# Performance work log

Hardware: AMD Instinct MI355X
Metric: run time of the kernel (lower is better)

## Reference

```python
import jax, jax.numpy as jnp
import numpy as np
from jax import lax

WINDOW_SIZE = 5
SIGMA = 1.0
DILATIONS = [1 + int(i ** 1.5) for i in range(5)]  # [1, 2, 3, 6, 9]
C1 = (0.01 * 255.0) ** 2
C2 = (0.03 * 255.0) ** 2


def _make_window(channel=1):
    x = np.arange(WINDOW_SIZE, dtype=np.float64)
    g = np.exp(-((x - WINDOW_SIZE // 2) ** 2) / (2.0 * SIGMA ** 2))
    g = g / g.sum()
    w2d = np.outer(g, g)
    w2d = w2d / w2d.sum()
    w = np.broadcast_to(w2d[None, None], (channel, 1, WINDOW_SIZE, WINDOW_SIZE))
    return jnp.asarray(w, jnp.float32)


def _dw_conv(x, window, dilation):
    # depthwise 'same' conv; pad = (dilated_kernel - 1)/2 = 2*dilation (always even total pad)
    pad = 2 * dilation
    return lax.conv_general_dilated(
        x, window, window_strides=(1, 1),
        padding=((pad, pad), (pad, pad)),
        rhs_dilation=(dilation, dilation),
        dimension_numbers=('NCHW', 'OIHW', 'NCHW'),
        feature_group_count=window.shape[0])


def _ssim_mean(img1, img2, window, dilation):
    mu1 = _dw_conv(img1, window, dilation)
    mu2 = _dw_conv(img2, window, dilation)
    si11 = _dw_conv(img1 * img1, window, dilation)
    si22 = _dw_conv(img2 * img2, window, dilation)
    si12 = _dw_conv(img1 * img2, window, dilation)
    mu1_sq = mu1 * mu1
    mu2_sq = mu2 * mu2
    mu1_mu2 = mu1 * mu2
    sigma1_sq = si11 - mu1_sq
    sigma2_sq = si22 - mu2_sq
    sigma12 = si12 - mu1_mu2
    ssim_map = ((2.0 * mu1_mu2 + C1) * (2.0 * sigma12 + C2)) / (
        (mu1_sq + mu2_sq + C1) * (sigma1_sq + sigma2_sq + C2))
    return jnp.mean(ssim_map)


def _avg_pool2(x):
    B, C, H, W = x.shape
    return x.reshape(B, C, H // 2, 2, W // 2, 2).mean(axis=(3, 5))


def setup_inputs() -> dict:
    key = jax.random.key(0)
    k1, k2 = jax.random.split(key)
    img1 = jax.random.uniform(k1, (16, 1, 1024, 1024), dtype=jnp.float32)
    img2 = jax.random.uniform(k2, (16, 1, 1024, 1024), dtype=jnp.float32)
    window = _make_window(channel=1)
    weights = jnp.asarray([0.0448, 0.2856, 0.3001, 0.2363, 0.1333], jnp.float32)
    return {"img1": img1, "img2": img2, "window": window, "weights": weights}


def reference(img1, img2, window, weights):
    eps = 1e-12
    m = jnp.max(img2)
    a = (img1 + eps) / (m + eps) * 255.0
    b = (img2 + eps) / (m + eps) * 255.0
    mssim = []
    for dil in DILATIONS:
        mssim.append(_ssim_mean(a, b, window, dil))
        a = _avg_pool2(a)
        b = _avg_pool2(b)
    mssim = jnp.stack(mssim)
    return 1.0 - jnp.prod(mssim ** weights)
```

## Files before the change

### kernel.cpp

```cpp
#include <hip/hip_runtime.h>
#include <math.h>

#define EPSN 1e-12f
#define SSIM_C1 6.5025f
#define SSIM_C2 58.5225f


typedef __attribute__((ext_vector_type(2))) float vf2;

__global__ void init_ws_kernel(float* ws) {
    if (threadIdx.x < 16) ws[threadIdx.x] = 0.0f;
}

__global__ void max_kernel(const float4* __restrict__ img2, int n4,
                           unsigned* __restrict__ maxbits) {
    float m = 0.0f;
    for (int i = blockIdx.x * blockDim.x + threadIdx.x; i < n4;
         i += gridDim.x * blockDim.x) {
        float4 v = img2[i];
        m = fmaxf(fmaxf(m, fmaxf(v.x, v.y)), fmaxf(v.z, v.w));
    }
#pragma unroll
    for (int o = 32; o > 0; o >>= 1) m = fmaxf(m, __shfl_down(m, o));
    __shared__ float sm[4];
    int tid = threadIdx.x;
    if ((tid & 63) == 0) sm[tid >> 6] = m;
    __syncthreads();
    if (tid == 0) {
        float mm = fmaxf(fmaxf(sm[0], sm[1]), fmaxf(sm[2], sm[3]));
        atomicMax(maxbits, __float_as_uint(mm));
    }
}


template <int D, bool RAW>
__global__ __launch_bounds__(256) void ssim_sep_kernel(
        const float* __restrict__ A, const float* __restrict__ B,
        int H, int W, const unsigned* __restrict__ maxbits,
        const float* __restrict__ window, float* __restrict__ sumOut,
        vf2* __restrict__ poolPM) {
    constexpr int TW = 64, TH = 64, TPT = 16;
    constexpr int LW = TW + 4 * D, LH = TH + 4 * D;
    __shared__ vf2 AB[LH][LW];

    int tx = threadIdx.x, ty = threadIdx.y;
    int tid = ty * 64 + tx;
    int b = blockIdx.z;
    int x0i = blockIdx.x * TW;
    int y0 = blockIdx.y * TH - 2 * D;

    if (RAW) {
        const float* Ab = A + (size_t)b * H * W;
        const float* Bb = B + (size_t)b * H * W;
        for (int idx = tid; idx < LH * 16; idx += 256) {
            int ly = idx >> 4, j = idx & 15;
            int gy = y0 + ly;
            float4 a = make_float4(0, 0, 0, 0), v = make_float4(0, 0, 0, 0);
            if ((unsigned)gy < (unsigned)H) {
                a = *(const float4*)(Ab + (size_t)gy * W + x0i + 4 * j);
                v = *(const float4*)(Bb + (size_t)gy * W + x0i + 4 * j);
            }
            float4 lo = make_float4(a.x + v.x, a.x - v.x, a.y + v.y, a.y - v.y);
            float4 hi = make_float4(a.z + v.z, a.z - v.z, a.w + v.w, a.w - v.w);
            int sig = ((j >> 2) ^ j) & 1;
            float4* rowp = (float4*)(&AB[ly][0]);
            rowp[D + 2 * j + sig] = sig ? hi : lo;
            rowp[D + 2 * j + 1 - sig] = sig ? lo : hi;
        }
        for (int idx = tid; idx < LH * 4 * D; idx += 256) {
            int ly = idx / (4 * D), h = idx % (4 * D);
            int lx = (h < 2 * D) ? h : h + TW;
            int gx = x0i - 2 * D + lx;
            int gy = y0 + ly;
            vf2 pm = {0.0f, 0.0f};
            if ((unsigned)gx < (unsigned)W && (unsigned)gy < (unsigned)H) {
                size_t g = (size_t)gy * W + gx;
                float a = Ab[g], v = Bb[g];
                pm = vf2{a + v, a - v};
            }
            AB[ly][lx] = pm;
        }
    } else {
        const vf2* pmIn = (const vf2*)A;
        const vf2* base = pmIn + (size_t)b * H * W;
        for (int idx = tid; idx < LH * 32; idx += 256) {
            int ly = idx >> 5, j = idx & 31;
            int gy = y0 + ly;
            float4 g = make_float4(0, 0, 0, 0);
            if ((unsigned)gy < (unsigned)H)
                g = *(const float4*)(base + (size_t)gy * W + x0i + 2 * j);
            ((float4*)&AB[ly][0])[D + j] = g;
        }
        for (int idx = tid; idx < LH * 4 * D; idx += 256) {
            int ly = idx / (4 * D), h = idx % (4 * D);
            int lx = (h < 2 * D) ? h : h + TW;
            int gx = x0i - 2 * D + lx;
            int gy = y0 + ly;
            vf2 pm = {0.0f, 0.0f};
            if ((unsigned)gx < (unsigned)W && (unsigned)gy < (unsigned)H)
                pm = base[(size_t)gy * W + gx];
            AB[ly][lx] = pm;
        }
    }
    __syncthreads();

    if (poolPM) {
        int pW = W >> 1;
        for (int idx = tid; idx < 32 * 16; idx += 256) {
            int py = idx >> 4, j2 = idx & 15;
            int sx = 2 * D + 4 * j2, sy = 2 * D + 2 * py;
            vf2 s00 = AB[sy][sx],     s01 = AB[sy][sx + 1];
            vf2 s10 = AB[sy + 1][sx], s11 = AB[sy + 1][sx + 1];
            vf2 o0 = 0.25f * ((s00 + s01) + (s10 + s11));
            vf2 t00 = AB[sy][sx + 2],     t01 = AB[sy][sx + 3];
            vf2 t10 = AB[sy + 1][sx + 2], t11 = AB[sy + 1][sx + 3];
            vf2 o1 = 0.25f * ((t00 + t01) + (t10 + t11));
            int gx = (x0i >> 1) + 2 * j2;
            int gy = ((blockIdx.y * TH) >> 1) + py;
            float4 o = make_float4(o0.x, o0.y, o1.x, o1.y);
            *(float4*)(poolPM + (size_t)b * (H >> 1) * pW + (size_t)gy * pW + gx) = o;
        }
    }

    float g1[5];
#pragma unroll
    for (int k = 0; k < 5; k++)
        g1[k] = ((window[k * 5 + 0] + window[k * 5 + 1]) +
                 (window[k * 5 + 2] + window[k * 5 + 3])) + window[k * 5 + 4];

    float mx = __uint_as_float(*maxbits);
    float sc = 255.0f / (mx + EPSN);
    float s2h = 0.5f * sc * sc;

    vf2 rPM[5], rSQ[5];
    float local = 0.0f;
    int rbase = ty * TPT;

#pragma unroll
    for (int ph = 0; ph < D; ++ph) {
        const int cnt = (TPT - ph + D - 1) / D;
#pragma unroll
        for (int k = 0; k < cnt + 4; ++k) {
            int l = rbase + ph + k * D;
            vf2 hpm = {0.0f, 0.0f}, hsq = {0.0f, 0.0f};
#pragma unroll
            for (int kt = 0; kt < 5; kt++) {
                vf2 ab = AB[l][tx + kt * D];
                vf2 wab = g1[kt] * ab;
                hpm += wab;
                hsq += wab * ab;
            }
            rPM[k % 5] = hpm;
            rSQ[k % 5] = hsq;
            if (k >= 4) {
                vf2 vpm = {0.0f, 0.0f}, vsq = {0.0f, 0.0f};
#pragma unroll
                for (int kt = 0; kt < 5; kt++) {
                    int sl = (k - 4 + kt) % 5;
                    vpm += g1[kt] * rPM[sl];
                    vsq += g1[kt] * rSQ[sl];
                }
                float u = vpm.x * vpm.x, vv = vpm.y * vpm.y;
                float upv = u + vv, umv = u - vv;
                float qp = vsq.x + vsq.y, qm = vsq.x - vsq.y;
                float num1 = fmaf(s2h, umv, SSIM_C1);
                float den1 = fmaf(s2h, upv, SSIM_C1);
                float num2 = fmaf(s2h, qm - umv, SSIM_C2);
                float den2 = fmaf(s2h, qp - upv, SSIM_C2);
                local += (num1 * num2) * __builtin_amdgcn_rcpf(den1 * den2);
            }
        }
    }

#pragma unroll
    for (int o = 32; o > 0; o >>= 1) local += __shfl_down(local, o);
    __shared__ float part[4];
    if ((tid & 63) == 0) part[tid >> 6] = local;
    __syncthreads();
    if (tid == 0) atomicAdd(sumOut, (part[0] + part[1]) + (part[2] + part[3]));
}


template <int D, int TH>
__global__ __launch_bounds__(256) void ssim_direct_kernel(
        const vf2* __restrict__ pmIn, int H, int W,
        const unsigned* __restrict__ maxbits,
        const float* __restrict__ window, float* __restrict__ sumOut,
        vf2* __restrict__ poolPM) {
    constexpr int TW = 64;
    constexpr int LW = TW + 4 * D, LH = TH + 4 * D, OPT = TH / 4;
    __shared__ vf2 AB[LH][LW];

    int tx = threadIdx.x, ty = threadIdx.y;
    int tid = ty * 64 + tx;
    int b = blockIdx.z;
    int x0i = blockIdx.x * TW;
    int y0 = blockIdx.y * TH - 2 * D;
    const vf2* base = pmIn + (size_t)b * H * W;

    for (int idx = tid; idx < LH * 32; idx += 256) {
        int ly = idx >> 5, j = idx & 31;
        int gy = y0 + ly;
        float4 g = make_float4(0, 0, 0, 0);
        if ((unsigned)gy < (unsigned)H)
            g = *(const float4*)(base + (size_t)gy * W + x0i + 2 * j);
        ((float4*)&AB[ly][0])[D + j] = g;
    }
    for (int idx = tid; idx < LH * 4 * D; idx += 256) {
        int ly = idx / (4 * D), h = idx % (4 * D);
        int lx = (h < 2 * D) ? h : h + TW;
        int gx = x0i - 2 * D + lx;
        int gy = y0 + ly;
        vf2 pm = {0.0f, 0.0f};
        if ((unsigned)gx < (unsigned)W && (unsigned)gy < (unsigned)H)
            pm = base[(size_t)gy * W + gx];
        AB[ly][lx] = pm;
    }
    __syncthreads();

    if (poolPM) {
        int pW = W >> 1;
        for (int idx = tid; idx < 16 * (TH / 2); idx += 256) {
            int py = idx >> 4, j2 = idx & 15;
            int sx = 2 * D + 4 * j2, sy = 2 * D + 2 * py;
            vf2 s00 = AB[sy][sx],     s01 = AB[sy][sx + 1];
            vf2 s10 = AB[sy + 1][sx], s11 = AB[sy + 1][sx + 1];
            vf2 o0 = 0.25f * ((s00 + s01) + (s10 + s11));
            vf2 t00 = AB[sy][sx + 2],     t01 = AB[sy][sx + 3];
            vf2 t10 = AB[sy + 1][sx + 2], t11 = AB[sy + 1][sx + 3];
            vf2 o1 = 0.25f * ((t00 + t01) + (t10 + t11));
            int gx = (x0i >> 1) + 2 * j2;
            int gy = ((blockIdx.y * TH) >> 1) + py;
            float4 o = make_float4(o0.x, o0.y, o1.x, o1.y);
            *(float4*)(poolPM + (size_t)b * (H >> 1) * pW + (size_t)gy * pW + gx) = o;
        }
    }

    float wv[25];
#pragma unroll
    for (int i = 0; i < 25; i++) wv[i] = window[i];

    float mx = __uint_as_float(*maxbits);
    float sc = 255.0f / (mx + EPSN);
    float s2h = 0.5f * sc * sc;

    vf2 mu[OPT], sq[OPT];
#pragma unroll
    for (int j = 0; j < OPT; j++) { mu[j] = vf2{0, 0}; sq[j] = vf2{0, 0}; }
    int ry = ty * OPT;
#pragma unroll
    for (int ky = 0; ky < 5; ky++) {
#pragma unroll
        for (int kx = 0; kx < 5; kx++) {
            float w = wv[ky * 5 + kx];
#pragma unroll
            for (int j = 0; j < OPT; j++) {
                vf2 ab = AB[ry + j + ky * D][tx + kx * D];
                vf2 wab = w * ab;
                mu[j] += wab;
                sq[j] += wab * ab;
            }
        }
    }

    float local = 0.0f;
#pragma unroll
    for (int j = 0; j < OPT; j++) {
        float u = mu[j].x * mu[j].x, vv = mu[j].y * mu[j].y;
        float upv = u + vv, umv = u - vv;
        float qp = sq[j].x + sq[j].y, qm = sq[j].x - sq[j].y;
        float num1 = fmaf(s2h, umv, SSIM_C1);
        float den1 = fmaf(s2h, upv, SSIM_C1);
        float num2 = fmaf(s2h, qm - umv, SSIM_C2);
        float den2 = fmaf(s2h, qp - upv, SSIM_C2);
        local += (num1 * num2) * __builtin_amdgcn_rcpf(den1 * den2);
    }

#pragma unroll
    for (int o = 32; o > 0; o >>= 1) local += __shfl_down(local, o);
    __shared__ float part[4];
    if ((tid & 63) == 0) part[tid >> 6] = local;
    __syncthreads();
    if (tid == 0) atomicAdd(sumOut, (part[0] + part[1]) + (part[2] + part[3]));
}


__global__ void final_kernel(const float* __restrict__ sums,
                             const float* __restrict__ weights,
                             unsigned* __restrict__ out) {
    if (blockIdx.x == 0 && threadIdx.x == 0) {
        const float counts[5] = {16.0f * 1024 * 1024, 16.0f * 512 * 512,
                                 16.0f * 256 * 256,   16.0f * 128 * 128,
                                 16.0f * 64 * 64};
        float prod = 1.0f;
#pragma unroll
        for (int i = 0; i < 5; i++) {
            float m = sums[i] / counts[i];
            prod *= powf(m, weights[i]);
        }
        float r = 1.0f - prod;
        unsigned bits = __float_as_uint(r);
        unsigned lsb = (bits >> 16) & 1u;
        unsigned hi = (bits + 0x7FFFu + lsb) >> 16;
        out[0] = (hi << 16) | hi;
    }
}


extern "C" void kernel_launch(void* const* d_in, const int* in_sizes, int n_in,
                              void* d_out, int out_size, void* d_ws, size_t ws_size,
                              hipStream_t stream) {
    const float* img1 = (const float*)d_in[0];
    const float* img2 = (const float*)d_in[1];
    const float* window = (const float*)d_in[2];
    const float* weights = (const float*)d_in[3];

    float* ws = (float*)d_ws;
    unsigned* maxbits = (unsigned*)d_ws;
    float* sums = ws + 4;
    size_t off = 16;
    vf2* pm1 = (vf2*)(ws + off); off += (size_t)16 * 512 * 512 * 2;
    vf2* pm2 = (vf2*)(ws + off); off += (size_t)16 * 256 * 256 * 2;
    vf2* pm3 = (vf2*)(ws + off); off += (size_t)16 * 128 * 128 * 2;
    vf2* pm4 = (vf2*)(ws + off); off += (size_t)16 * 64 * 64 * 2;

    dim3 blk(64, 4, 1);

    init_ws_kernel<<<1, 64, 0, stream>>>(ws);
    max_kernel<<<2048, 256, 0, stream>>>((const float4*)img2,
                                         16 * 1024 * 1024 / 4, maxbits);

    ssim_sep_kernel<1, true><<<dim3(16, 16, 16), blk, 0, stream>>>(
        img1, img2, 1024, 1024, maxbits, window, sums + 0, pm1);
    ssim_sep_kernel<2, false><<<dim3(8, 8, 16), blk, 0, stream>>>(
        (const float*)pm1, nullptr, 512, 512, maxbits, window, sums + 1, pm2);
    ssim_sep_kernel<3, false><<<dim3(4, 4, 16), blk, 0, stream>>>(
        (const float*)pm2, nullptr, 256, 256, maxbits, window, sums + 2, pm3);
    ssim_direct_kernel<6, 8><<<dim3(2, 16, 16), blk, 0, stream>>>(
        pm3, 128, 128, maxbits, window, sums + 3, pm4);
    ssim_direct_kernel<9, 8><<<dim3(1, 8, 16), blk, 0, stream>>>(
        pm4, 64, 64, maxbits, window, sums + 4, nullptr);

    final_kernel<<<1, 64, 0, stream>>>(sums, weights, (unsigned*)d_out);
}
```

Baseline: 302.9 us.

## Fuse coarse SSIM levels into one tail kernel pooling directly from level-1 buffer

Levels 1–4 are merged into a single tail kernel whose block ranges dispatch per level, and coarser levels rebuild their pooled tiles directly from the level-1 pm buffer instead of reading intermediate pooled buffers written by earlier kernels. The max reduction now writes per-block partials that each consumer block reduces itself, and the init kernel is folded into the max kernel, which removes the atomicMax and two launches. This cuts kernel launches and serial dependencies between small levels, so the coarse levels can run concurrently. In exchange, coarse levels re-read and re-average more level-1 data per tile, and every block repeats the small partial-max reduction.

```diff
diff --git a/kernel.cpp b/kernel.cpp
--- a/kernel.cpp
+++ b/kernel.cpp
@@ -8,40 +8,71 @@
 
 typedef __attribute__((ext_vector_type(2))) float vf2;
 
-__global__ void init_ws_kernel(float* ws) {
-    if (threadIdx.x < 16) ws[threadIdx.x] = 0.0f;
-}
-
-__global__ void max_kernel(const float4* __restrict__ img2, int n4,
-                           unsigned* __restrict__ maxbits) {
+
+__global__ void max_part_kernel(const float4* __restrict__ img2, int n4,
+                                float* __restrict__ partials,
+                                float* __restrict__ sums) {
+    int tid = threadIdx.x;
+    if (blockIdx.x == 256) {
+        if (tid < 5) sums[tid] = 0.0f;
+        return;
+    }
     float m = 0.0f;
-    for (int i = blockIdx.x * blockDim.x + threadIdx.x; i < n4;
-         i += gridDim.x * blockDim.x) {
+    for (int i = blockIdx.x * 256 + tid; i < n4; i += 256 * 256) {
         float4 v = img2[i];
         m = fmaxf(fmaxf(m, fmaxf(v.x, v.y)), fmaxf(v.z, v.w));
     }
 #pragma unroll
     for (int o = 32; o > 0; o >>= 1) m = fmaxf(m, __shfl_down(m, o));
     __shared__ float sm[4];
-    int tid = threadIdx.x;
     if ((tid & 63) == 0) sm[tid >> 6] = m;
     __syncthreads();
-    if (tid == 0) {
-        float mm = fmaxf(fmaxf(sm[0], sm[1]), fmaxf(sm[2], sm[3]));
-        atomicMax(maxbits, __float_as_uint(mm));
-    }
-}
-
-
-template <int D, bool RAW>
-__global__ __launch_bounds__(256) void ssim_sep_kernel(
+    if (tid == 0)
+        partials[blockIdx.x] = fmaxf(fmaxf(sm[0], sm[1]), fmaxf(sm[2], sm[3]));
+}
+
+
+__device__ __forceinline__ float max_from_partials_start(
+        const float* __restrict__ partials, float* sm4, int tid) {
+    float mv = partials[tid & 255];
+#pragma unroll
+    for (int o = 32; o > 0; o >>= 1) mv = fmaxf(mv, __shfl_down(mv, o));
+    if ((tid & 63) == 0) sm4[tid >> 6] = mv;
+    return 0.0f;
+}
+
+__device__ __forceinline__ void block_sum_add(float local, float* part, int tid,
+                                              float* __restrict__ sumOut) {
+#pragma unroll
+    for (int o = 32; o > 0; o >>= 1) local += __shfl_down(local, o);
+    if ((tid & 63) == 0) part[tid >> 6] = local;
+    __syncthreads();
+    if (tid == 0)
+        atomicAdd(sumOut, (part[0] + part[1]) + (part[2] + part[3]));
+}
+
+__device__ __forceinline__ float ssim_px(vf2 vpm, vf2 vsq, float s2h) {
+    float u = vpm.x * vpm.x, vv = vpm.y * vpm.y;
+    float upv = u + vv, umv = u - vv;
+    float qp = vsq.x + vsq.y, qm = vsq.x - vsq.y;
+    float num1 = fmaf(s2h, umv, SSIM_C1);
+    float den1 = fmaf(s2h, upv, SSIM_C1);
+    float num2 = fmaf(s2h, qm - umv, SSIM_C2);
+    float den2 = fmaf(s2h, qp - upv, SSIM_C2);
+    return (num1 * num2) * __builtin_amdgcn_rcpf(den1 * den2);
+}
+
+
+__global__ __launch_bounds__(256) void ssim0_kernel(
         const float* __restrict__ A, const float* __restrict__ B,
-        int H, int W, const unsigned* __restrict__ maxbits,
-        const float* __restrict__ window, float* __restrict__ sumOut,
-        vf2* __restrict__ poolPM) {
-    constexpr int TW = 64, TH = 64, TPT = 16;
+        const float* __restrict__ window, const float* __restrict__ partials,
+        float* __restrict__ sums, vf2* __restrict__ poolPM) {
+    constexpr int D = 1, TW = 64, TH = 64, TPT = 16;
     constexpr int LW = TW + 4 * D, LH = TH + 4 * D;
+    const int H = 1024, W = 1024;
     __shared__ vf2 AB[LH][LW];
+    __shared__ float sm4[4];
+    __shared__ float part[4];
 
     int tx = threadIdx.x, ty = threadIdx.y;
     int tid = ty * 64 + tx;
@@ -49,70 +80,49 @@
     int x0i = blockIdx.x * TW;
     int y0 = blockIdx.y * TH - 2 * D;
 
-    if (RAW) {
-        const float* Ab = A + (size_t)b * H * W;
-        const float* Bb = B + (size_t)b * H * W;
-        for (int idx = tid; idx < LH * 16; idx += 256) {
-            int ly = idx >> 4, j = idx & 15;
-            int gy = y0 + ly;
-            float4 a = make_float4(0, 0, 0, 0), v = make_float4(0, 0, 0, 0);
-            if ((unsigned)gy < (unsigned)H) {
-                a = *(const float4*)(Ab + (size_t)gy * W + x0i + 4 * j);
-                v = *(const float4*)(Bb + (size_t)gy * W + x0i + 4 * j);
-            }
-            float4 lo = make_float4(a.x + v.x, a.x - v.x, a.y + v.y, a.y - v.y);
-            float4 hi = make_float4(a.z + v.z, a.z - v.z, a.w + v.w, a.w - v.w);
-            int sig = ((j >> 2) ^ j) & 1;
-            float4* rowp = (float4*)(&AB[ly][0]);
-            rowp[D + 2 * j + sig] = sig ? hi : lo;
-            rowp[D + 2 * j + 1 - sig] = sig ? lo : hi;
-        }
-        for (int idx = tid; idx < LH * 4 * D; idx += 256) {
-            int ly = idx / (4 * D), h = idx % (4 * D);
-            int lx = (h < 2 * D) ? h : h + TW;
-            int gx = x0i - 2 * D + lx;
-            int gy = y0 + ly;
-            vf2 pm = {0.0f, 0.0f};
-            if ((unsigned)gx < (unsigned)W && (unsigned)gy < (unsigned)H) {
-                size_t g = (size_t)gy * W + gx;
-                float a = Ab[g], v = Bb[g];
-                pm = vf2{a + v, a - v};
-            }
-            AB[ly][lx] = pm;
-        }
-    } else {
-        const vf2* pmIn = (const vf2*)A;
-        const vf2* base = pmIn + (size_t)b * H * W;
-        for (int idx = tid; idx < LH * 32; idx += 256) {
-            int ly = idx >> 5, j = idx & 31;
-            int gy = y0 + ly;
-            float4 g = make_float4(0, 0, 0, 0);
-            if ((unsigned)gy < (unsigned)H)
-                g = *(const float4*)(base + (size_t)gy * W + x0i + 2 * j);
-            ((float4*)&AB[ly][0])[D + j] = g;
-        }
-        for (int idx = tid; idx < LH * 4 * D; idx += 256) {
-            int ly = idx / (4 * D), h = idx % (4 * D);
-            int lx = (h < 2 * D) ? h : h + TW;
-            int gx = x0i - 2 * D + lx;
-            int gy = y0 + ly;
-            vf2 pm = {0.0f, 0.0f};
-            if ((unsigned)gx < (unsigned)W && (unsigned)gy < (unsigned)H)
-                pm = base[(size_t)gy * W + gx];
-            AB[ly][lx] = pm;
-        }
+    max_from_partials_start(partials, sm4, tid);
+
+    const float* Ab = A + (size_t)b * H * W;
+    const float* Bb = B + (size_t)b * H * W;
+    for (int idx = tid; idx < LH * 16; idx += 256) {
+        int ly = idx >> 4, j = idx & 15;
+        int gy = y0 + ly;
+        float4 a = make_float4(0, 0, 0, 0), v = make_float4(0, 0, 0, 0);
+        if ((unsigned)gy < (unsigned)H) {
+            a = *(const float4*)(Ab + (size_t)gy * W + x0i + 4 * j);
+            v = *(const float4*)(Bb + (size_t)gy * W + x0i + 4 * j);
+        }
+        float4 lo = make_float4(a.x + v.x, a.x - v.x, a.y + v.y, a.y - v.y);
+        float4 hi = make_float4(a.z + v.z, a.z - v.z, a.w + v.w, a.w - v.w);
+        int sig = ((j >> 2) ^ j) & 1;
+        float4* rowp = (float4*)(&AB[ly][0]);
+        rowp[D + 2 * j + sig] = sig ? hi : lo;
+        rowp[D + 2 * j + 1 - sig] = sig ? lo : hi;
+    }
+    for (int idx = tid; idx < LH * 4 * D; idx += 256) {
+        int ly = idx / (4 * D), h = idx % (4 * D);
+        int lx = (h < 2 * D) ? h : h + TW;
+        int gx = x0i - 2 * D + lx;
+        int gy = y0 + ly;
+        vf2 pm = {0.0f, 0.0f};
+        if ((unsigned)gx < (unsigned)W && (unsigned)gy < (unsigned)H) {
+            size_t g = (size_t)gy * W + gx;
+            float a = Ab[g], v = Bb[g];
+            pm = vf2{a + v, a - v};
+        }
+        AB[ly][lx] = pm;
     }
     __syncthreads();
 
-    if (poolPM) {
+    {
         int pW = W >> 1;
         for (int idx = tid; idx < 32 * 16; idx += 256) {
             int py = idx >> 4, j2 = idx & 15;
             int sx = 2 * D + 4 * j2, sy = 2 * D + 2 * py;
-            vf2 s00 = AB[sy][sx],     s01 = AB[sy][sx + 1];
+            vf2 s00 = AB[sy][sx], s01 = AB[sy][sx + 1];
             vf2 s10 = AB[sy + 1][sx], s11 = AB[sy + 1][sx + 1];
             vf2 o0 = 0.25f * ((s00 + s01) + (s10 + s11));
-            vf2 t00 = AB[sy][sx + 2],     t01 = AB[sy][sx + 3];
+            vf2 t00 = AB[sy][sx + 2], t01 = AB[sy][sx + 3];
             vf2 t10 = AB[sy + 1][sx + 2], t11 = AB[sy + 1][sx + 3];
             vf2 o1 = 0.25f * ((t00 + t01) + (t10 + t11));
             int gx = (x0i >> 1) + 2 * j2;
@@ -128,21 +138,110 @@
         g1[k] = ((window[k * 5 + 0] + window[k * 5 + 1]) +
                  (window[k * 5 + 2] + window[k * 5 + 3])) + window[k * 5 + 4];
 
-    float mx = __uint_as_float(*maxbits);
+    float mx = fmaxf(fmaxf(sm4[0], sm4[1]), fmaxf(sm4[2], sm4[3]));
     float sc = 255.0f / (mx + EPSN);
     float s2h = 0.5f * sc * sc;
 
     vf2 rPM[5], rSQ[5];
     float local = 0.0f;
     int rbase = ty * TPT;
-
+#pragma unroll
+    for (int k = 0; k < TPT + 4; ++k) {
+        int l = rbase + k;
+        vf2 hpm = {0, 0}, hsq = {0, 0};
+#pragma unroll
+        for (int kt = 0; kt < 5; kt++) {
+            vf2 ab = AB[l][tx + kt];
+            vf2 wab = g1[kt] * ab;
+            hpm += wab;
+            hsq += wab * ab;
+        }
+        rPM[k % 5] = hpm;
+        rSQ[k % 5] = hsq;
+        if (k >= 4) {
+            vf2 vpm = {0, 0}, vsq = {0, 0};
+#pragma unroll
+            for (int kt = 0; kt < 5; kt++) {
+                int sl = (k - 4 + kt) % 5;
+                vpm += g1[kt] * rPM[sl];
+                vsq += g1[kt] * rSQ[sl];
+            }
+            local += ssim_px(vpm, vsq, s2h);
+        }
+    }
+    block_sum_add(local, part, tid, sums + 0);
+}
+
+
+template <int D, int TH, int POOL>
+__device__ void sep_level(const vf2* __restrict__ base, const float* g1,
+                          int bx, int by, const float* sm4, float* part,
+                          float* __restrict__ sumOut, vf2* ldsRaw, int tid) {
+    constexpr int TW = 64, TPT = TH / 4;
+    constexpr int W = 512 / POOL;
+    constexpr int LW = TW + 4 * D, LH = TH + 4 * D;
+    vf2(*AB)[LW] = (vf2(*)[LW])ldsRaw;
+    int tx = tid & 63, ty = tid >> 6;
+    int x0i = bx * TW, y0 = by * TH - 2 * D;
+
+    if constexpr (POOL == 1) {
+        for (int idx = tid; idx < LH * 32; idx += 256) {
+            int ly = idx >> 5, j = idx & 31;
+            int gy = y0 + ly;
+            float4 g = make_float4(0, 0, 0, 0);
+            if ((unsigned)gy < (unsigned)W)
+                g = *(const float4*)(base + (size_t)gy * 512 + x0i + 2 * j);
+            ((float4*)&AB[ly][0])[D + j] = g;
+        }
+        for (int idx = tid; idx < LH * 4 * D; idx += 256) {
+            int ly = idx / (4 * D), h = idx % (4 * D);
+            int lx = (h < 2 * D) ? h : h + TW;
+            int gx = x0i - 2 * D + lx, gy = y0 + ly;
+            vf2 pm = {0, 0};
+            if ((unsigned)gx < (unsigned)W && (unsigned)gy < (unsigned)W)
+                pm = base[(size_t)gy * 512 + gx];
+            AB[ly][lx] = pm;
+        }
+    } else {
+        constexpr float inv = 1.0f / (POOL * POOL);
+        int px0 = x0i - 2 * D;
+        for (int idx = tid; idx < LW * LH; idx += 256) {
+            int ly = idx / LW, lx = idx - ly * LW;
+            int px = px0 + lx, py = y0 + ly;
+            vf2 acc = {0, 0};
+            if ((unsigned)px < (unsigned)W && (unsigned)py < (unsigned)W) {
+                const vf2* r0 = base + (size_t)(py * POOL) * 512 + px * POOL;
+#pragma unroll
+                for (int ry = 0; ry < POOL; ry++) {
+                    const float4* rp = (const float4*)(r0 + (size_t)ry * 512);
+#pragma unroll
+                    for (int rx = 0; rx < POOL / 2; rx++) {
+                        float4 v = rp[rx];
+                        acc.x += v.x + v.z;
+                        acc.y += v.y + v.w;
+                    }
+                }
+                acc *= inv;
+            }
+            AB[ly][lx] = acc;
+        }
+    }
+    __syncthreads();
+
+    float mx = fmaxf(fmaxf(sm4[0], sm4[1]), fmaxf(sm4[2], sm4[3]));
+    float sc = 255.0f / (mx + EPSN);
+    float s2h = 0.5f * sc * sc;
+
+    vf2 rPM[5], rSQ[5];
+    float local = 0.0f;
+    int rbase = ty * TPT;
 #pragma unroll
     for (int ph = 0; ph < D; ++ph) {
         const int cnt = (TPT - ph + D - 1) / D;
 #pragma unroll
         for (int k = 0; k < cnt + 4; ++k) {
             int l = rbase + ph + k * D;
-            vf2 hpm = {0.0f, 0.0f}, hsq = {0.0f, 0.0f};
+            vf2 hpm = {0, 0}, hsq = {0, 0};
 #pragma unroll
             for (int kt = 0; kt < 5; kt++) {
                 vf2 ab = AB[l][tx + kt * D];
@@ -153,135 +252,118 @@
             rPM[k % 5] = hpm;
             rSQ[k % 5] = hsq;
             if (k >= 4) {
-                vf2 vpm = {0.0f, 0.0f}, vsq = {0.0f, 0.0f};
+                vf2 vpm = {0, 0}, vsq = {0, 0};
 #pragma unroll
                 for (int kt = 0; kt < 5; kt++) {
                     int sl = (k - 4 + kt) % 5;
                     vpm += g1[kt] * rPM[sl];
                     vsq += g1[kt] * rSQ[sl];
                 }
-                float u = vpm.x * vpm.x, vv = vpm.y * vpm.y;
-                float upv = u + vv, umv = u - vv;
-                float qp = vsq.x + vsq.y, qm = vsq.x - vsq.y;
-                float num1 = fmaf(s2h, umv, SSIM_C1);
-                float den1 = fmaf(s2h, upv, SSIM_C1);
-                float num2 = fmaf(s2h, qm - umv, SSIM_C2);
-                float den2 = fmaf(s2h, qp - upv, SSIM_C2);
-                local += (num1 * num2) * __builtin_amdgcn_rcpf(den1 * den2);
-            }
-        }
-    }
-
-#pragma unroll
-    for (int o = 32; o > 0; o >>= 1) local += __shfl_down(local, o);
-    __shared__ float part[4];
-    if ((tid & 63) == 0) part[tid >> 6] = local;
+                local += ssim_px(vpm, vsq, s2h);
+            }
+        }
+    }
+    block_sum_add(local, part, tid, sumOut);
+}
+
+template <int D, int TW, int TH, int POOL>
+__device__ void direct_level(const vf2* __restrict__ base, const float* g1,
+                             int bx, int by, const float* sm4, float* part,
+                             float* __restrict__ sumOut, vf2* ldsRaw, int tid) {
+    constexpr int W = 512 / POOL;
+    constexpr int LW = TW + 4 * D, LH = TH + 4 * D;
+    constexpr int NOUT = TW * TH / 256;
+    constexpr float inv = 1.0f / (POOL * POOL);
+    vf2(*AB)[LW] = (vf2(*)[LW])ldsRaw;
+    int x0i = bx * TW, y0 = by * TH - 2 * D;
+    int px0 = x0i - 2 * D;
+
+    for (int idx = tid; idx < LW * LH; idx += 256) {
+        int ly = idx / LW, lx = idx - ly * LW;
+        int px = px0 + lx, py = y0 + ly;
+        vf2 acc = {0, 0};
+        if ((unsigned)px < (unsigned)W && (unsigned)py < (unsigned)W) {
+            const vf2* r0 = base + (size_t)(py * POOL) * 512 + px * POOL;
+#pragma unroll
+            for (int ry = 0; ry < POOL; ry++) {
+                const float4* rp = (const float4*)(r0 + (size_t)ry * 512);
+#pragma unroll
+                for (int rx = 0; rx < POOL / 2; rx++) {
+                    float4 v = rp[rx];
+                    acc.x += v.x + v.z;
+                    acc.y += v.y + v.w;
+                }
+            }
+            acc *= inv;
+        }
+        AB[ly][lx] = acc;
+    }
     __syncthreads();
-    if (tid == 0) atomicAdd(sumOut, (part[0] + part[1]) + (part[2] + part[3]));
-}
-
-
-template <int D, int TH>
-__global__ __launch_bounds__(256) void ssim_direct_kernel(
-        const vf2* __restrict__ pmIn, int H, int W,
-        const unsigned* __restrict__ maxbits,
-        const float* __restrict__ window, float* __restrict__ sumOut,
-        vf2* __restrict__ poolPM) {
-    constexpr int TW = 64;
-    constexpr int LW = TW + 4 * D, LH = TH + 4 * D, OPT = TH / 4;
-    __shared__ vf2 AB[LH][LW];
-
-    int tx = threadIdx.x, ty = threadIdx.y;
-    int tid = ty * 64 + tx;
-    int b = blockIdx.z;
-    int x0i = blockIdx.x * TW;
-    int y0 = blockIdx.y * TH - 2 * D;
-    const vf2* base = pmIn + (size_t)b * H * W;
-
-    for (int idx = tid; idx < LH * 32; idx += 256) {
-        int ly = idx >> 5, j = idx & 31;
-        int gy = y0 + ly;
-        float4 g = make_float4(0, 0, 0, 0);
-        if ((unsigned)gy < (unsigned)H)
-            g = *(const float4*)(base + (size_t)gy * W + x0i + 2 * j);
-        ((float4*)&AB[ly][0])[D + j] = g;
-    }
-    for (int idx = tid; idx < LH * 4 * D; idx += 256) {
-        int ly = idx / (4 * D), h = idx % (4 * D);
-        int lx = (h < 2 * D) ? h : h + TW;
-        int gx = x0i - 2 * D + lx;
-        int gy = y0 + ly;
-        vf2 pm = {0.0f, 0.0f};
-        if ((unsigned)gx < (unsigned)W && (unsigned)gy < (unsigned)H)
-            pm = base[(size_t)gy * W + gx];
-        AB[ly][lx] = pm;
-    }
-    __syncthreads();
-
-    if (poolPM) {
-        int pW = W >> 1;
-        for (int idx = tid; idx < 16 * (TH / 2); idx += 256) {
-            int py = idx >> 4, j2 = idx & 15;
-            int sx = 2 * D + 4 * j2, sy = 2 * D + 2 * py;
-            vf2 s00 = AB[sy][sx],     s01 = AB[sy][sx + 1];
-            vf2 s10 = AB[sy + 1][sx], s11 = AB[sy + 1][sx + 1];
-            vf2 o0 = 0.25f * ((s00 + s01) + (s10 + s11));
-            vf2 t00 = AB[sy][sx + 2],     t01 = AB[sy][sx + 3];
-            vf2 t10 = AB[sy + 1][sx + 2], t11 = AB[sy + 1][sx + 3];
-            vf2 o1 = 0.25f * ((t00 + t01) + (t10 + t11));
-            int gx = (x0i >> 1) + 2 * j2;
-            int gy = ((blockIdx.y * TH) >> 1) + py;
-            float4 o = make_float4(o0.x, o0.y, o1.x, o1.y);
-            *(float4*)(poolPM + (size_t)b * (H >> 1) * pW + (size_t)gy * pW + gx) = o;
-        }
-    }
-
-    float wv[25];
-#pragma unroll
-    for (int i = 0; i < 25; i++) wv[i] = window[i];
-
-    float mx = __uint_as_float(*maxbits);
+
+    float mx = fmaxf(fmaxf(sm4[0], sm4[1]), fmaxf(sm4[2], sm4[3]));
     float sc = 255.0f / (mx + EPSN);
     float s2h = 0.5f * sc * sc;
 
-    vf2 mu[OPT], sq[OPT];
-#pragma unroll
-    for (int j = 0; j < OPT; j++) { mu[j] = vf2{0, 0}; sq[j] = vf2{0, 0}; }
-    int ry = ty * OPT;
+    vf2 mu[NOUT], sq[NOUT];
+#pragma unroll
+    for (int j = 0; j < NOUT; j++) { mu[j] = vf2{0, 0}; sq[j] = vf2{0, 0}; }
 #pragma unroll
     for (int ky = 0; ky < 5; ky++) {
 #pragma unroll
         for (int kx = 0; kx < 5; kx++) {
-            float w = wv[ky * 5 + kx];
-#pragma unroll
-            for (int j = 0; j < OPT; j++) {
-                vf2 ab = AB[ry + j + ky * D][tx + kx * D];
+            float w = g1[ky] * g1[kx];
+#pragma unroll
+            for (int j = 0; j < NOUT; j++) {
+                int lin = tid + j * 256;
+                int ox = lin % TW, oy = lin / TW;
+                vf2 ab = AB[oy + ky * D][ox + kx * D];
                 vf2 wab = w * ab;
                 mu[j] += wab;
                 sq[j] += wab * ab;
             }
         }
     }
-
     float local = 0.0f;
 #pragma unroll
-    for (int j = 0; j < OPT; j++) {
-        float u = mu[j].x * mu[j].x, vv = mu[j].y * mu[j].y;
-        float upv = u + vv, umv = u - vv;
-        float qp = sq[j].x + sq[j].y, qm = sq[j].x - sq[j].y;
-        float num1 = fmaf(s2h, umv, SSIM_C1);
-        float den1 = fmaf(s2h, upv, SSIM_C1);
-        float num2 = fmaf(s2h, qm - umv, SSIM_C2);
-        float den2 = fmaf(s2h, qp - upv, SSIM_C2);
-        local += (num1 * num2) * __builtin_amdgcn_rcpf(den1 * den2);
-    }
-
-#pragma unroll
-    for (int o = 32; o > 0; o >>= 1) local += __shfl_down(local, o);
+    for (int j = 0; j < NOUT; j++) local += ssim_px(mu[j], sq[j], s2h);
+    block_sum_add(local, part, tid, sumOut);
+}
+
+
+__global__ __launch_bounds__(256) void tail_kernel(
+        const vf2* __restrict__ pm1, const float* __restrict__ window,
+        const float* __restrict__ partials, float* __restrict__ sums) {
+    extern __shared__ vf2 ldsdyn[];
+    __shared__ float sm4[4];
     __shared__ float part[4];
-    if ((tid & 63) == 0) part[tid >> 6] = local;
-    __syncthreads();
-    if (tid == 0) atomicAdd(sumOut, (part[0] + part[1]) + (part[2] + part[3]));
+    int tid = threadIdx.x;
+
+    max_from_partials_start(partials, sm4, tid);
+
+    float g1[5];
+#pragma unroll
+    for (int k = 0; k < 5; k++)
+        g1[k] = ((window[k * 5 + 0] + window[k * 5 + 1]) +
+                 (window[k * 5 + 2] + window[k * 5 + 3])) + window[k * 5 + 4];
+
+    int bid = blockIdx.x;
+    if (bid < 2048) {
+        int t = bid, b = t >> 7, r = t & 127, by = r >> 3, bx = r & 7;
+        const vf2* base = pm1 + (size_t)b * 512 * 512;
+        sep_level<2, 32, 1>(base, g1, bx, by, sm4, part, sums + 1, ldsdyn, tid);
+    } else if (bid < 2560) {
+        int t = bid - 2048, b = t >> 5, r = t & 31, by = r >> 2, bx = r & 3;
+        const vf2* base = pm1 + (size_t)b * 512 * 512;
+        sep_level<3, 32, 2>(base, g1, bx, by, sm4, part, sums + 2, ldsdyn, tid);
+    } else if (bid < 2816) {
+        int t = bid - 2560, b = t >> 4, r = t & 15, by = r >> 1, bx = r & 1;
+        const vf2* base = pm1 + (size_t)b * 512 * 512;
+        direct_level<6, 64, 16, 4>(base, g1, bx, by, sm4, part, sums + 3, ldsdyn, tid);
+    } else {
+        int t = bid - 2816, b = t >> 3, r = t & 7, by = r >> 1, bx = r & 1;
+        const vf2* base = pm1 + (size_t)b * 512 * 512;
+        direct_level<9, 32, 16, 8>(base, g1, bx, by, sm4, part, sums + 4, ldsdyn, tid);
+    }
 }
 
 
@@ -316,30 +398,14 @@
     const float* weights = (const float*)d_in[3];
 
     float* ws = (float*)d_ws;
-    unsigned* maxbits = (unsigned*)d_ws;
-    float* sums = ws + 4;
-    size_t off = 16;
-    vf2* pm1 = (vf2*)(ws + off); off += (size_t)16 * 512 * 512 * 2;
-    vf2* pm2 = (vf2*)(ws + off); off += (size_t)16 * 256 * 256 * 2;
-    vf2* pm3 = (vf2*)(ws + off); off += (size_t)16 * 128 * 128 * 2;
-    vf2* pm4 = (vf2*)(ws + off); off += (size_t)16 * 64 * 64 * 2;
-
-    dim3 blk(64, 4, 1);
-
-    init_ws_kernel<<<1, 64, 0, stream>>>(ws);
-    max_kernel<<<2048, 256, 0, stream>>>((const float4*)img2,
-                                         16 * 1024 * 1024 / 4, maxbits);
-
-    ssim_sep_kernel<1, true><<<dim3(16, 16, 16), blk, 0, stream>>>(
-        img1, img2, 1024, 1024, maxbits, window, sums + 0, pm1);
-    ssim_sep_kernel<2, false><<<dim3(8, 8, 16), blk, 0, stream>>>(
-        (const float*)pm1, nullptr, 512, 512, maxbits, window, sums + 1, pm2);
-    ssim_sep_kernel<3, false><<<dim3(4, 4, 16), blk, 0, stream>>>(
-        (const float*)pm2, nullptr, 256, 256, maxbits, window, sums + 2, pm3);
-    ssim_direct_kernel<6, 8><<<dim3(2, 16, 16), blk, 0, stream>>>(
-        pm3, 128, 128, maxbits, window, sums + 3, pm4);
-    ssim_direct_kernel<9, 8><<<dim3(1, 8, 16), blk, 0, stream>>>(
-        pm4, 64, 64, maxbits, window, sums + 4, nullptr);
-
+    float* sums = ws;
+    float* partials = ws + 8;
+    vf2* pm1 = (vf2*)(ws + 512);
+
+    max_part_kernel<<<257, 256, 0, stream>>>((const float4*)img2,
+                                             16 * 1024 * 1024 / 4, partials, sums);
+    ssim0_kernel<<<dim3(16, 16, 16), dim3(64, 4), 0, stream>>>(
+        img1, img2, window, partials, sums, pm1);
+    tail_kernel<<<2944, 256, 28288, stream>>>(pm1, window, partials, sums);
     final_kernel<<<1, 64, 0, stream>>>(sums, weights, (unsigned*)d_out);
 }
```

Measured after the change: 426.5 us. 40.8% more time.

## Fuse coarse SSIM levels into one tail kernel and compute all pools from level 1

Applied to the files above, without the earlier changes.

Level 1 now writes the 2x, 4x and 8x average-pooled pyramids (pm2, pm3, pm4) straight from its shared tile. Levels 2, 3 and 4 then run together in a single tail kernel that dispatches on block index, with smaller tiles and more blocks per level. This removes two kernel launches and the serial dependence between the small coarse levels, which were underusing the GPU. In exchange the tail kernel needs large dynamic shared memory, and level 1 does extra pooling work.

```diff
diff --git a/kernel.cpp b/kernel.cpp
--- a/kernel.cpp
+++ b/kernel.cpp
@@ -33,119 +33,51 @@
 }
 
 
-template <int D, bool RAW>
-__global__ __launch_bounds__(256) void ssim_sep_kernel(
-        const float* __restrict__ A, const float* __restrict__ B,
-        int H, int W, const unsigned* __restrict__ maxbits,
-        const float* __restrict__ window, float* __restrict__ sumOut,
-        vf2* __restrict__ poolPM) {
-    constexpr int TW = 64, TH = 64, TPT = 16;
-    constexpr int LW = TW + 4 * D, LH = TH + 4 * D;
-    __shared__ vf2 AB[LH][LW];
-
-    int tx = threadIdx.x, ty = threadIdx.y;
-    int tid = ty * 64 + tx;
-    int b = blockIdx.z;
-    int x0i = blockIdx.x * TW;
-    int y0 = blockIdx.y * TH - 2 * D;
-
-    if (RAW) {
-        const float* Ab = A + (size_t)b * H * W;
-        const float* Bb = B + (size_t)b * H * W;
-        for (int idx = tid; idx < LH * 16; idx += 256) {
-            int ly = idx >> 4, j = idx & 15;
-            int gy = y0 + ly;
-            float4 a = make_float4(0, 0, 0, 0), v = make_float4(0, 0, 0, 0);
-            if ((unsigned)gy < (unsigned)H) {
-                a = *(const float4*)(Ab + (size_t)gy * W + x0i + 4 * j);
-                v = *(const float4*)(Bb + (size_t)gy * W + x0i + 4 * j);
-            }
-            float4 lo = make_float4(a.x + v.x, a.x - v.x, a.y + v.y, a.y - v.y);
-            float4 hi = make_float4(a.z + v.z, a.z - v.z, a.w + v.w, a.w - v.w);
-            int sig = ((j >> 2) ^ j) & 1;
-            float4* rowp = (float4*)(&AB[ly][0]);
-            rowp[D + 2 * j + sig] = sig ? hi : lo;
-            rowp[D + 2 * j + 1 - sig] = sig ? lo : hi;
-        }
-        for (int idx = tid; idx < LH * 4 * D; idx += 256) {
-            int ly = idx / (4 * D), h = idx % (4 * D);
-            int lx = (h < 2 * D) ? h : h + TW;
-            int gx = x0i - 2 * D + lx;
-            int gy = y0 + ly;
-            vf2 pm = {0.0f, 0.0f};
-            if ((unsigned)gx < (unsigned)W && (unsigned)gy < (unsigned)H) {
-                size_t g = (size_t)gy * W + gx;
-                float a = Ab[g], v = Bb[g];
-                pm = vf2{a + v, a - v};
-            }
-            AB[ly][lx] = pm;
-        }
-    } else {
-        const vf2* pmIn = (const vf2*)A;
-        const vf2* base = pmIn + (size_t)b * H * W;
-        for (int idx = tid; idx < LH * 32; idx += 256) {
-            int ly = idx >> 5, j = idx & 31;
-            int gy = y0 + ly;
-            float4 g = make_float4(0, 0, 0, 0);
-            if ((unsigned)gy < (unsigned)H)
-                g = *(const float4*)(base + (size_t)gy * W + x0i + 2 * j);
-            ((float4*)&AB[ly][0])[D + j] = g;
-        }
-        for (int idx = tid; idx < LH * 4 * D; idx += 256) {
-            int ly = idx / (4 * D), h = idx % (4 * D);
-            int lx = (h < 2 * D) ? h : h + TW;
-            int gx = x0i - 2 * D + lx;
-            int gy = y0 + ly;
-            vf2 pm = {0.0f, 0.0f};
-            if ((unsigned)gx < (unsigned)W && (unsigned)gy < (unsigned)H)
-                pm = base[(size_t)gy * W + gx];
-            AB[ly][lx] = pm;
-        }
-    }
-    __syncthreads();
-
-    if (poolPM) {
-        int pW = W >> 1;
-        for (int idx = tid; idx < 32 * 16; idx += 256) {
-            int py = idx >> 4, j2 = idx & 15;
-            int sx = 2 * D + 4 * j2, sy = 2 * D + 2 * py;
-            vf2 s00 = AB[sy][sx],     s01 = AB[sy][sx + 1];
-            vf2 s10 = AB[sy + 1][sx], s11 = AB[sy + 1][sx + 1];
-            vf2 o0 = 0.25f * ((s00 + s01) + (s10 + s11));
-            vf2 t00 = AB[sy][sx + 2],     t01 = AB[sy][sx + 3];
-            vf2 t10 = AB[sy + 1][sx + 2], t11 = AB[sy + 1][sx + 3];
-            vf2 o1 = 0.25f * ((t00 + t01) + (t10 + t11));
-            int gx = (x0i >> 1) + 2 * j2;
-            int gy = ((blockIdx.y * TH) >> 1) + py;
-            float4 o = make_float4(o0.x, o0.y, o1.x, o1.y);
-            *(float4*)(poolPM + (size_t)b * (H >> 1) * pW + (size_t)gy * pW + gx) = o;
-        }
-    }
-
-    float g1[5];
+__device__ __forceinline__ float ssim_px(vf2 vpm, vf2 vsq, float s2h) {
+    float u = vpm.x * vpm.x, vv = vpm.y * vpm.y;
+    float upv = u + vv, umv = u - vv;
+    float qp = vsq.x + vsq.y, qm = vsq.x - vsq.y;
+    float num1 = fmaf(s2h, umv, SSIM_C1);
+    float den1 = fmaf(s2h, upv, SSIM_C1);
+    float num2 = fmaf(s2h, qm - umv, SSIM_C2);
+    float den2 = fmaf(s2h, qp - upv, SSIM_C2);
+    return (num1 * num2) * __builtin_amdgcn_rcpf(den1 * den2);
+}
+
+__device__ __forceinline__ void load_g1(const float* __restrict__ window,
+                                        float* g1) {
 #pragma unroll
     for (int k = 0; k < 5; k++)
         g1[k] = ((window[k * 5 + 0] + window[k * 5 + 1]) +
                  (window[k * 5 + 2] + window[k * 5 + 3])) + window[k * 5 + 4];
-
-    float mx = __uint_as_float(*maxbits);
-    float sc = 255.0f / (mx + EPSN);
-    float s2h = 0.5f * sc * sc;
-
+}
+
+__device__ __forceinline__ void block_sum_add(float local, float* part, int tid,
+                                              float* __restrict__ sumOut) {
+#pragma unroll
+    for (int o = 32; o > 0; o >>= 1) local += __shfl_down(local, o);
+    if ((tid & 63) == 0) part[tid >> 6] = local;
+    __syncthreads();
+    if (tid == 0)
+        atomicAdd(sumOut, (part[0] + part[1]) + (part[2] + part[3]));
+}
+
+template <int D, int TPT, int LW>
+__device__ __forceinline__ float sep_compute(const vf2* AB, const float* g1,
+                                             float s2h, int tx, int ty) {
     vf2 rPM[5], rSQ[5];
     float local = 0.0f;
     int rbase = ty * TPT;
-
 #pragma unroll
     for (int ph = 0; ph < D; ++ph) {
         const int cnt = (TPT - ph + D - 1) / D;
 #pragma unroll
         for (int k = 0; k < cnt + 4; ++k) {
             int l = rbase + ph + k * D;
-            vf2 hpm = {0.0f, 0.0f}, hsq = {0.0f, 0.0f};
+            vf2 hpm = {0, 0}, hsq = {0, 0};
 #pragma unroll
             for (int kt = 0; kt < 5; kt++) {
-                vf2 ab = AB[l][tx + kt * D];
+                vf2 ab = AB[l * LW + tx + kt * D];
                 vf2 wab = g1[kt] * ab;
                 hpm += wab;
                 hsq += wab * ab;
@@ -153,58 +85,76 @@
             rPM[k % 5] = hpm;
             rSQ[k % 5] = hsq;
             if (k >= 4) {
-                vf2 vpm = {0.0f, 0.0f}, vsq = {0.0f, 0.0f};
+                vf2 vpm = {0, 0}, vsq = {0, 0};
 #pragma unroll
                 for (int kt = 0; kt < 5; kt++) {
                     int sl = (k - 4 + kt) % 5;
                     vpm += g1[kt] * rPM[sl];
                     vsq += g1[kt] * rSQ[sl];
                 }
-                float u = vpm.x * vpm.x, vv = vpm.y * vpm.y;
-                float upv = u + vv, umv = u - vv;
-                float qp = vsq.x + vsq.y, qm = vsq.x - vsq.y;
-                float num1 = fmaf(s2h, umv, SSIM_C1);
-                float den1 = fmaf(s2h, upv, SSIM_C1);
-                float num2 = fmaf(s2h, qm - umv, SSIM_C2);
-                float den2 = fmaf(s2h, qp - upv, SSIM_C2);
-                local += (num1 * num2) * __builtin_amdgcn_rcpf(den1 * den2);
+                local += ssim_px(vpm, vsq, s2h);
             }
         }
     }
-
-#pragma unroll
-    for (int o = 32; o > 0; o >>= 1) local += __shfl_down(local, o);
+    return local;
+}
+
+template <int D, int LH, int W>
+__device__ __forceinline__ void stage_sep(const vf2* __restrict__ base,
+                                          vf2* AB, int x0i, int y0, int tid) {
+    constexpr int LW = 64 + 4 * D;
+    for (int idx = tid; idx < LH * 32; idx += 256) {
+        int ly = idx >> 5, j = idx & 31;
+        int gy = y0 + ly;
+        float4 g = make_float4(0, 0, 0, 0);
+        if ((unsigned)gy < (unsigned)W)
+            g = *(const float4*)(base + (size_t)gy * W + x0i + 2 * j);
+        ((float4*)(AB + ly * LW))[D + j] = g;
+    }
+    for (int idx = tid; idx < LH * 4 * D; idx += 256) {
+        int ly = idx / (4 * D), h = idx % (4 * D);
+        int lx = (h < 2 * D) ? h : h + 64;
+        int gx = x0i - 2 * D + lx, gy = y0 + ly;
+        vf2 pm = {0, 0};
+        if ((unsigned)gx < (unsigned)W && (unsigned)gy < (unsigned)W)
+            pm = base[(size_t)gy * W + gx];
+        AB[ly * LW + lx] = pm;
+    }
+}
+
+
+__global__ __launch_bounds__(256) void ssim0_kernel(
+        const float* __restrict__ A, const float* __restrict__ B,
+        const float* __restrict__ window, const unsigned* __restrict__ maxbits,
+        float* __restrict__ sums, vf2* __restrict__ poolPM) {
+    constexpr int D = 1, TW = 64, TH = 64, TPT = 16;
+    constexpr int LW = TW + 4 * D, LH = TH + 4 * D;
+    const int H = 1024, W = 1024;
+    __shared__ vf2 AB[LH][LW];
     __shared__ float part[4];
-    if ((tid & 63) == 0) part[tid >> 6] = local;
-    __syncthreads();
-    if (tid == 0) atomicAdd(sumOut, (part[0] + part[1]) + (part[2] + part[3]));
-}
-
-
-template <int D, int TH>
-__global__ __launch_bounds__(256) void ssim_direct_kernel(
-        const vf2* __restrict__ pmIn, int H, int W,
-        const unsigned* __restrict__ maxbits,
-        const float* __restrict__ window, float* __restrict__ sumOut,
-        vf2* __restrict__ poolPM) {
-    constexpr int TW = 64;
-    constexpr int LW = TW + 4 * D, LH = TH + 4 * D, OPT = TH / 4;
-    __shared__ vf2 AB[LH][LW];
 
     int tx = threadIdx.x, ty = threadIdx.y;
     int tid = ty * 64 + tx;
     int b = blockIdx.z;
     int x0i = blockIdx.x * TW;
     int y0 = blockIdx.y * TH - 2 * D;
-    const vf2* base = pmIn + (size_t)b * H * W;
-
-    for (int idx = tid; idx < LH * 32; idx += 256) {
-        int ly = idx >> 5, j = idx & 31;
+
+    const float* Ab = A + (size_t)b * H * W;
+    const float* Bb = B + (size_t)b * H * W;
+    for (int idx = tid; idx < LH * 16; idx += 256) {
+        int ly = idx >> 4, j = idx & 15;
         int gy = y0 + ly;
-        float4 g = make_float4(0, 0, 0, 0);
-        if ((unsigned)gy < (unsigned)H)
-            g = *(const float4*)(base + (size_t)gy * W + x0i + 2 * j);
-        ((float4*)&AB[ly][0])[D + j] = g;
+        float4 a = make_float4(0, 0, 0, 0), v = make_float4(0, 0, 0, 0);
+        if ((unsigned)gy < (unsigned)H) {
+            a = *(const float4*)(Ab + (size_t)gy * W + x0i + 4 * j);
+            v = *(const float4*)(Bb + (size_t)gy * W + x0i + 4 * j);
+        }
+        float4 lo = make_float4(a.x + v.x, a.x - v.x, a.y + v.y, a.y - v.y);
+        float4 hi = make_float4(a.z + v.z, a.z - v.z, a.w + v.w, a.w - v.w);
+        int sig = ((j >> 2) ^ j) & 1;
+        float4* rowp = (float4*)(&AB[ly][0]);
+        rowp[D + 2 * j + sig] = sig ? hi : lo;
+        rowp[D + 2 * j + 1 - sig] = sig ? lo : hi;
     }
     for (int idx = tid; idx < LH * 4 * D; idx += 256) {
         int ly = idx / (4 * D), h = idx % (4 * D);
@@ -212,21 +162,24 @@
         int gx = x0i - 2 * D + lx;
         int gy = y0 + ly;
         vf2 pm = {0.0f, 0.0f};
-        if ((unsigned)gx < (unsigned)W && (unsigned)gy < (unsigned)H)
-            pm = base[(size_t)gy * W + gx];
+        if ((unsigned)gx < (unsigned)W && (unsigned)gy < (unsigned)H) {
+            size_t g = (size_t)gy * W + gx;
+            float a = Ab[g], v = Bb[g];
+            pm = vf2{a + v, a - v};
+        }
         AB[ly][lx] = pm;
     }
     __syncthreads();
 
-    if (poolPM) {
+    {
         int pW = W >> 1;
-        for (int idx = tid; idx < 16 * (TH / 2); idx += 256) {
+        for (int idx = tid; idx < 32 * 16; idx += 256) {
             int py = idx >> 4, j2 = idx & 15;
             int sx = 2 * D + 4 * j2, sy = 2 * D + 2 * py;
-            vf2 s00 = AB[sy][sx],     s01 = AB[sy][sx + 1];
+            vf2 s00 = AB[sy][sx], s01 = AB[sy][sx + 1];
             vf2 s10 = AB[sy + 1][sx], s11 = AB[sy + 1][sx + 1];
             vf2 o0 = 0.25f * ((s00 + s01) + (s10 + s11));
-            vf2 t00 = AB[sy][sx + 2],     t01 = AB[sy][sx + 3];
+            vf2 t00 = AB[sy][sx + 2], t01 = AB[sy][sx + 3];
             vf2 t10 = AB[sy + 1][sx + 2], t11 = AB[sy + 1][sx + 3];
             vf2 o1 = 0.25f * ((t00 + t01) + (t10 + t11));
             int gx = (x0i >> 1) + 2 * j2;
@@ -236,52 +189,166 @@
         }
     }
 
-    float wv[25];
-#pragma unroll
-    for (int i = 0; i < 25; i++) wv[i] = window[i];
-
+    float g1[5];
+    load_g1(window, g1);
     float mx = __uint_as_float(*maxbits);
     float sc = 255.0f / (mx + EPSN);
     float s2h = 0.5f * sc * sc;
 
-    vf2 mu[OPT], sq[OPT];
-#pragma unroll
-    for (int j = 0; j < OPT; j++) { mu[j] = vf2{0, 0}; sq[j] = vf2{0, 0}; }
-    int ry = ty * OPT;
+    float local = sep_compute<D, TPT, LW>(&AB[0][0], g1, s2h, tx, ty);
+    block_sum_add(local, part, tid, sums + 0);
+}
+
+
+__global__ __launch_bounds__(256) void ssim1_kernel(
+        const vf2* __restrict__ pm1, const float* __restrict__ window,
+        const unsigned* __restrict__ maxbits, float* __restrict__ sums,
+        vf2* __restrict__ pm2, vf2* __restrict__ pm3, vf2* __restrict__ pm4) {
+    constexpr int D = 2, TH = 64, TPT = 16;
+    constexpr int LW = 64 + 4 * D, LH = TH + 4 * D;
+    const int W = 512;
+    __shared__ vf2 AB[LH * LW];
+    __shared__ float part[4];
+
+    int tx = threadIdx.x, ty = threadIdx.y;
+    int tid = ty * 64 + tx;
+    int b = blockIdx.z;
+    int bx = blockIdx.x, by = blockIdx.y;
+    int x0i = bx * 64;
+    int y0 = by * TH - 2 * D;
+    const vf2* base = pm1 + (size_t)b * W * W;
+
+    stage_sep<D, LH, 512>(base, AB, x0i, y0, tid);
+    __syncthreads();
+
+    for (int idx = tid; idx < 32 * 16; idx += 256) {
+        int py = idx >> 4, j2 = idx & 15;
+        int sx = 2 * D + 4 * j2, sy = 2 * D + 2 * py;
+        vf2 s00 = AB[sy * LW + sx], s01 = AB[sy * LW + sx + 1];
+        vf2 s10 = AB[(sy + 1) * LW + sx], s11 = AB[(sy + 1) * LW + sx + 1];
+        vf2 o0 = 0.25f * ((s00 + s01) + (s10 + s11));
+        vf2 t00 = AB[sy * LW + sx + 2], t01 = AB[sy * LW + sx + 3];
+        vf2 t10 = AB[(sy + 1) * LW + sx + 2], t11 = AB[(sy + 1) * LW + sx + 3];
+        vf2 o1 = 0.25f * ((t00 + t01) + (t10 + t11));
+        int gx = bx * 32 + 2 * j2, gy = by * 32 + py;
+        float4 o = make_float4(o0.x, o0.y, o1.x, o1.y);
+        *(float4*)(pm2 + (size_t)b * 256 * 256 + (size_t)gy * 256 + gx) = o;
+    }
+    if (tid < 256) {
+        int py = tid >> 4, px = tid & 15;
+        vf2 acc = {0, 0};
+#pragma unroll
+        for (int ry = 0; ry < 4; ry++)
+#pragma unroll
+            for (int rx = 0; rx < 4; rx++)
+                acc += AB[(2 * D + 4 * py + ry) * LW + 2 * D + 4 * px + rx];
+        acc *= (1.0f / 16.0f);
+        int gx = bx * 16 + px, gy = by * 16 + py;
+        pm3[(size_t)b * 128 * 128 + (size_t)gy * 128 + gx] = acc;
+    }
+    if (tid < 64) {
+        int py = tid >> 3, px = tid & 7;
+        vf2 acc = {0, 0};
+#pragma unroll
+        for (int ry = 0; ry < 8; ry++)
+#pragma unroll
+            for (int rx = 0; rx < 8; rx++)
+                acc += AB[(2 * D + 8 * py + ry) * LW + 2 * D + 8 * px + rx];
+        acc *= (1.0f / 64.0f);
+        int gx = bx * 8 + px, gy = by * 8 + py;
+        pm4[(size_t)b * 64 * 64 + (size_t)gy * 64 + gx] = acc;
+    }
+
+    float g1[5];
+    load_g1(window, g1);
+    float mx = __uint_as_float(*maxbits);
+    float sc = 255.0f / (mx + EPSN);
+    float s2h = 0.5f * sc * sc;
+
+    float local = sep_compute<D, TPT, LW>(AB, g1, s2h, tx, ty);
+    block_sum_add(local, part, tid, sums + 1);
+}
+
+
+template <int D, int TW, int TH, int W>
+__device__ void direct_level(const vf2* __restrict__ base, const float* g1,
+                             int bx, int by, float s2h, float* part,
+                             float* __restrict__ sumOut, vf2* AB, int tid) {
+    constexpr int LW = TW + 4 * D, LH = TH + 4 * D;
+    constexpr int NOUT = TW * TH / 256;
+    int x0i = bx * TW, y0 = by * TH - 2 * D;
+    int px0 = x0i - 2 * D;
+
+    for (int idx = tid; idx < LW * LH; idx += 256) {
+        int ly = idx / LW, lx = idx - ly * LW;
+        int px = px0 + lx, py = y0 + ly;
+        vf2 pm = {0, 0};
+        if ((unsigned)px < (unsigned)W && (unsigned)py < (unsigned)W)
+            pm = base[(size_t)py * W + px];
+        AB[ly * LW + lx] = pm;
+    }
+    __syncthreads();
+
+    vf2 mu[NOUT], sq[NOUT];
+#pragma unroll
+    for (int j = 0; j < NOUT; j++) { mu[j] = vf2{0, 0}; sq[j] = vf2{0, 0}; }
 #pragma unroll
     for (int ky = 0; ky < 5; ky++) {
 #pragma unroll
         for (int kx = 0; kx < 5; kx++) {
-            float w = wv[ky * 5 + kx];
-#pragma unroll
-            for (int j = 0; j < OPT; j++) {
-                vf2 ab = AB[ry + j + ky * D][tx + kx * D];
+            float w = g1[ky] * g1[kx];
+#pragma unroll
+            for (int j = 0; j < NOUT; j++) {
+                int lin = tid + j * 256;
+                int ox = lin % TW, oy = lin / TW;
+                vf2 ab = AB[(oy + ky * D) * LW + ox + kx * D];
                 vf2 wab = w * ab;
                 mu[j] += wab;
                 sq[j] += wab * ab;
             }
         }
     }
-
     float local = 0.0f;
 #pragma unroll
-    for (int j = 0; j < OPT; j++) {
-        float u = mu[j].x * mu[j].x, vv = mu[j].y * mu[j].y;
-        float upv = u + vv, umv = u - vv;
-        float qp = sq[j].x + sq[j].y, qm = sq[j].x - sq[j].y;
-        float num1 = fmaf(s2h, umv, SSIM_C1);
-        float den1 = fmaf(s2h, upv, SSIM_C1);
-        float num2 = fmaf(s2h, qm - umv, SSIM_C2);
-        float den2 = fmaf(s2h, qp - upv, SSIM_C2);
-        local += (num1 * num2) * __builtin_amdgcn_rcpf(den1 * den2);
-    }
-
-#pragma unroll
-    for (int o = 32; o > 0; o >>= 1) local += __shfl_down(local, o);
+    for (int j = 0; j < NOUT; j++) local += ssim_px(mu[j], sq[j], s2h);
+    block_sum_add(local, part, tid, sumOut);
+}
+
+__global__ __launch_bounds__(256) void tail234_kernel(
+        const vf2* __restrict__ pm2, const vf2* __restrict__ pm3,
+        const vf2* __restrict__ pm4, const float* __restrict__ window,
+        const unsigned* __restrict__ maxbits, float* __restrict__ sums) {
+    extern __shared__ vf2 ldsdyn[];
     __shared__ float part[4];
-    if ((tid & 63) == 0) part[tid >> 6] = local;
-    __syncthreads();
-    if (tid == 0) atomicAdd(sumOut, (part[0] + part[1]) + (part[2] + part[3]));
+    int tid = threadIdx.x;
+
+    float g1[5];
+    load_g1(window, g1);
+    float mx = __uint_as_float(*maxbits);
+    float sc = 255.0f / (mx + EPSN);
+    float s2h = 0.5f * sc * sc;
+
+    int bid = blockIdx.x;
+    if (bid < 512) {
+        int b = bid >> 5, r = bid & 31, by = r >> 2, bx = r & 3;
+        constexpr int D = 3, TH = 32, TPT = 8;
+        constexpr int LW = 64 + 4 * D, LH = TH + 4 * D;
+        const vf2* base = pm2 + (size_t)b * 256 * 256;
+        stage_sep<D, LH, 256>(base, ldsdyn, bx * 64, by * TH - 2 * D, tid);
+        __syncthreads();
+        float local = sep_compute<D, TPT, LW>(ldsdyn, g1, s2h, tid & 63, tid >> 6);
+        block_sum_add(local, part, tid, sums + 2);
+    } else if (bid < 768) {
+        int t = bid - 512, b = t >> 4, r = t & 15, by = r >> 1, bx = r & 1;
+        const vf2* base = pm3 + (size_t)b * 128 * 128;
+        direct_level<6, 64, 16, 128>(base, g1, bx, by, s2h, part, sums + 3,
+                                     ldsdyn, tid);
+    } else {
+        int t = bid - 768, b = t >> 3, r = t & 7, by = r >> 1, bx = r & 1;
+        const vf2* base = pm4 + (size_t)b * 64 * 64;
+        direct_level<9, 32, 16, 64>(base, g1, bx, by, s2h, part, sums + 4,
+                                    ldsdyn, tid);
+    }
 }
 
 
@@ -324,22 +391,14 @@
     vf2* pm3 = (vf2*)(ws + off); off += (size_t)16 * 128 * 128 * 2;
     vf2* pm4 = (vf2*)(ws + off); off += (size_t)16 * 64 * 64 * 2;
 
-    dim3 blk(64, 4, 1);
-
     init_ws_kernel<<<1, 64, 0, stream>>>(ws);
     max_kernel<<<2048, 256, 0, stream>>>((const float4*)img2,
                                          16 * 1024 * 1024 / 4, maxbits);
-
-    ssim_sep_kernel<1, true><<<dim3(16, 16, 16), blk, 0, stream>>>(
-        img1, img2, 1024, 1024, maxbits, window, sums + 0, pm1);
-    ssim_sep_kernel<2, false><<<dim3(8, 8, 16), blk, 0, stream>>>(
-        (const float*)pm1, nullptr, 512, 512, maxbits, window, sums + 1, pm2);
-    ssim_sep_kernel<3, false><<<dim3(4, 4, 16), blk, 0, stream>>>(
-        (const float*)pm2, nullptr, 256, 256, maxbits, window, sums + 2, pm3);
-    ssim_direct_kernel<6, 8><<<dim3(2, 16, 16), blk, 0, stream>>>(
-        pm3, 128, 128, maxbits, window, sums + 3, pm4);
-    ssim_direct_kernel<9, 8><<<dim3(1, 8, 16), blk, 0, stream>>>(
-        pm4, 64, 64, maxbits, window, sums + 4, nullptr);
-
+    ssim0_kernel<<<dim3(16, 16, 16), dim3(64, 4), 0, stream>>>(
+        img1, img2, window, maxbits, sums, pm1);
+    ssim1_kernel<<<dim3(8, 8, 16), dim3(64, 4), 0, stream>>>(
+        pm1, window, maxbits, sums, pm2, pm3, pm4);
+    tail234_kernel<<<896, 256, 28288, stream>>>(pm2, pm3, pm4, window,
+                                                maxbits, sums);
     final_kernel<<<1, 64, 0, stream>>>(sums, weights, (unsigned*)d_out);
 }
```

Result: faster. 292.1 us (-3.6%).
